# Kernel tuning notes

Measured on AMD Instinct MI355X. Metric: run time of the kernel, lower is better.

The kernel has to match this reference:

```python
import jax, jax.numpy as jnp
import numpy as np

HEADS = 8
DIM_HEAD = 64
SCALE = DIM_HEAD ** -0.5


def setup_inputs() -> dict:
    key = jax.random.key(0)
    ks = jax.random.split(key, 6)
    b, n, d = 2, 4096, 1024
    inner = HEADS * DIM_HEAD  # 512
    x = jax.random.normal(ks[0], (b, n, d), dtype=jnp.float32)
    Wq = jax.random.normal(ks[1], (d, inner), dtype=jnp.float32) * (d ** -0.5)
    Wk = jax.random.normal(ks[2], (d, inner), dtype=jnp.float32) * (d ** -0.5)
    Wv = jax.random.normal(ks[3], (d, inner), dtype=jnp.float32) * (d ** -0.5)
    Wout = jax.random.normal(ks[4], (inner, d), dtype=jnp.float32) * (inner ** -0.5)
    bout = jnp.zeros((d,), dtype=jnp.float32)
    return {"x": x, "Wq": Wq, "Wk": Wk, "Wv": Wv, "Wout": Wout, "bout": bout}


def reference(x, Wq, Wk, Wv, Wout, bout):
    b, n, _ = x.shape
    h, dh = HEADS, DIM_HEAD
    # self-attention: context = x
    q = (x @ Wq).reshape(b, n, h, dh).transpose(0, 2, 1, 3)  # b h n d
    k = (x @ Wk).reshape(b, n, h, dh).transpose(0, 2, 1, 3)
    v = (x @ Wv).reshape(b, n, h, dh).transpose(0, 2, 1, 3)
    sim = jnp.einsum('bhid,bhjd->bhij', q, k) * SCALE  # full score matrix
    attn = jax.nn.softmax(sim, axis=-1)
    out = jnp.einsum('bhij,bhjd->bhid', attn, v)
    out = out.transpose(0, 2, 1, 3).reshape(b, n, h * dh)  # b n (h d)
    return out @ Wout + bout
```

## Files before the change

### kernel.cpp

```cpp
#include <hip/hip_runtime.h>
#include <hip/hip_bf16.h>

typedef __bf16 bf16x8 __attribute__((ext_vector_type(8)));
typedef __bf16 bf16x4 __attribute__((ext_vector_type(4)));
typedef float floatx4 __attribute__((ext_vector_type(4)));

#define MFMA16(a, b, c) __builtin_amdgcn_mfma_f32_16x16x32_bf16((a), (b), (c), 0, 0, 0)

__device__ __forceinline__ void stage16(const __bf16* g, __bf16* lds_base) {
  __builtin_amdgcn_global_load_lds(
      (__attribute__((address_space(1))) void*)(void*)g,
      (__attribute__((address_space(3))) void*)lds_base, 16, 0, 0);
}

__global__ void detect_dtype(const unsigned int* __restrict__ x, int* __restrict__ flag) {
  __shared__ int cnt;
  if (threadIdx.x == 0) cnt = 0;
  __syncthreads();
  int c = 0;
  for (int i = threadIdx.x; i < 4096; i += 256) {
    const unsigned f = (x[i] >> 7) & 0xFF;
    c += (f >= 100 && f <= 140) ? 1 : 0;
  }
  atomicAdd(&cnt, c);
  __syncthreads();
  if (threadIdx.x == 0) *flag = (cnt > 2048) ? 1 : 0;
}

__global__ __launch_bounds__(256) void convert_x(const void* __restrict__ src,
                                                 __bf16* __restrict__ dst,
                                                 const int* __restrict__ flagp) {
  const int isbf = *flagp;
  const size_t i = ((size_t)blockIdx.x * 256 + threadIdx.x) * 8;
  if (isbf) {
    *(bf16x8*)(dst + i) = *(const bf16x8*)((const __bf16*)src + i);
  } else {
    const float4 f0 = *(const float4*)((const float*)src + i);
    const float4 f1 = *(const float4*)((const float*)src + i + 4);
    bf16x8 v;
    v[0] = (__bf16)f0.x; v[1] = (__bf16)f0.y; v[2] = (__bf16)f0.z; v[3] = (__bf16)f0.w;
    v[4] = (__bf16)f1.x; v[5] = (__bf16)f1.y; v[6] = (__bf16)f1.z; v[7] = (__bf16)f1.w;
    *(bf16x8*)(dst + i) = v;
  }
}

__global__ __launch_bounds__(256) void transpose3_conv(
    const void* __restrict__ s0, const void* __restrict__ s1,
    const void* __restrict__ s2, __bf16* __restrict__ dst,
    int R, int C, const int* __restrict__ flagp) {
  __shared__ __bf16 t[32][33];
  const int isbf = *flagp;
  const void* src = (blockIdx.z == 0) ? s0 : (blockIdx.z == 1) ? s1 : s2;
  __bf16* d = dst + (size_t)blockIdx.z * R * C;
  const int bx = blockIdx.x * 32, by = blockIdx.y * 32;
  const int x = threadIdx.x & 31, y0 = threadIdx.x >> 5;
#pragma unroll
  for (int i = y0; i < 32; i += 8) {
    const size_t idx = (size_t)(by + i) * C + bx + x;
    t[i][x] = isbf ? ((const __bf16*)src)[idx] : (__bf16)(((const float*)src)[idx]);
  }
  __syncthreads();
#pragma unroll
  for (int i = y0; i < 32; i += 8) d[(size_t)(bx + i) * R + by + x] = t[x][i];
}

__global__ __launch_bounds__(256) void transpose_conv(const void* __restrict__ src,
                                                      __bf16* __restrict__ dst,
                                                      int R, int C,
                                                      const int* __restrict__ flagp) {
  __shared__ __bf16 t[32][33];
  const int isbf = *flagp;
  const int bx = blockIdx.x * 32, by = blockIdx.y * 32;
  const int x = threadIdx.x & 31, y0 = threadIdx.x >> 5;
#pragma unroll
  for (int i = y0; i < 32; i += 8) {
    const size_t idx = (size_t)(by + i) * C + bx + x;
    t[i][x] = isbf ? ((const __bf16*)src)[idx] : (__bf16)(((const float*)src)[idx]);
  }
  __syncthreads();
#pragma unroll
  for (int i = y0; i < 32; i += 8) dst[(size_t)(bx + i) * R + by + x] = t[x][i];
}

__global__ __launch_bounds__(256) void vp_transpose(const __bf16* __restrict__ V,
                                                    __bf16* __restrict__ VP) {
  alignas(16) __shared__ __bf16 t[64][64];
  const int bh = blockIdx.y, s0 = blockIdx.x * 64;
  const int row = threadIdx.x >> 2, part = threadIdx.x & 3;
  const __bf16* src = V + (size_t)bh * 262144 + (size_t)(s0 + row) * 64 + part * 16;
  *(bf16x8*)&t[row][part * 16] = *(const bf16x8*)src;
  *(bf16x8*)&t[row][part * 16 + 8] = *(const bf16x8*)(src + 8);
  __syncthreads();
  const int d = row, og = part;
  bf16x8 w0, w1;
#pragma unroll
  for (int e = 0; e < 8; e++) {
    const int o0 = og * 16 + e, o1 = og * 16 + 8 + e;
    w0[e] = t[(o0 & 3) * 16 + (o0 >> 2)][d];
    w1[e] = t[(o1 & 3) * 16 + (o1 >> 2)][d];
  }
  __bf16* dst = VP + (size_t)bh * 262144 + (size_t)d * 4096 + s0 + og * 16;
  *(bf16x8*)dst = w0;
  *(bf16x8*)(dst + 8) = w1;
}

__global__ __launch_bounds__(256) void gemm_bt(
    const __bf16* __restrict__ A, const __bf16* __restrict__ Bt,
    void* __restrict__ Cv, void* __restrict__ Cv2, int M, int N, int K,
    const void* __restrict__ bias, int permute, int egress_dual,
    size_t zsB, size_t zsC, const int* __restrict__ flagp) {
  alignas(16) __shared__ __bf16 As[128 * 32];
  alignas(16) __shared__ __bf16 Bs[128 * 32];
  const int isbf = *flagp;
  Bt += blockIdx.z * zsB;
  const size_t zoff = (size_t)blockIdx.z * zsC;
  const int tid = threadIdx.x;
  const int wave = tid >> 6, lane = tid & 63;
  const int m0 = blockIdx.y * 128, n0 = blockIdx.x * 128;
  const int wm = (wave & 1) * 64, wn = (wave >> 1) * 64;
  const int fr = lane & 15, fq = lane >> 4;

  const floatx4 zero4 = {0.f, 0.f, 0.f, 0.f};
  floatx4 acc[4][4];
#pragma unroll
  for (int i = 0; i < 4; i++)
#pragma unroll
    for (int j = 0; j < 4; j++) acc[i][j] = zero4;

  const int lrow = lane >> 2;
  const int lk = (lane & 3) * 8;

  for (int k0 = 0; k0 < K; k0 += 32) {
#pragma unroll
    for (int cc = 0; cc < 2; ++cc) {
      const int c = 2 * wave + cc;
      stage16(A + (size_t)(m0 + c * 16 + lrow) * K + k0 + lk, &As[c * 512]);
      stage16(Bt + (size_t)(n0 + c * 16 + lrow) * K + k0 + lk, &Bs[c * 512]);
    }
    __syncthreads();
    bf16x8 af[4], bg[4];
#pragma unroll
    for (int mt = 0; mt < 4; mt++)
      af[mt] = *(const bf16x8*)&As[(wm + mt * 16 + fr) * 32 + fq * 8];
#pragma unroll
    for (int nt = 0; nt < 4; nt++)
      bg[nt] = *(const bf16x8*)&Bs[(wn + nt * 16 + fr) * 32 + fq * 8];
#pragma unroll
    for (int mt = 0; mt < 4; mt++)
#pragma unroll
      for (int nt = 0; nt < 4; nt++)
        acc[mt][nt] = MFMA16(af[mt], bg[nt], acc[mt][nt]);
    __syncthreads();
  }

  const float qs = (permute && blockIdx.z == 0) ? 0.18033688011112042f
                                                : 1.0f;
#pragma unroll
  for (int mt = 0; mt < 4; mt++)
#pragma unroll
    for (int nt = 0; nt < 4; nt++)
#pragma unroll
      for (int r = 0; r < 4; r++) {
        const int row = m0 + wm + mt * 16 + fq * 4 + r;
        const int col = n0 + wn + nt * 16 + fr;
        float v = acc[mt][nt][r] * qs;
        if (bias)
          v += isbf ? (float)((const __bf16*)bias)[col] : ((const float*)bias)[col];
        if (permute) {
          const int bh = (row >> 12) * 8 + (col >> 6);
          const int s = row & 4095, d = col & 63;
          const size_t pidx = (size_t)bh * 262144 + (size_t)s * 64 + d;
          if (blockIdx.z == 2)
            ((__bf16*)Cv2)[pidx] = (__bf16)v;
          else
            ((__bf16*)Cv)[zoff + pidx] = (__bf16)v;
        } else {
          const size_t idx = (size_t)row * N + col;
          if (egress_dual && !isbf)
            ((float*)Cv)[idx] = v;
          else
            ((__bf16*)Cv)[idx] = (__bf16)v;
        }
      }
}

#define ATT_S 4096
#define KV_SPLIT 2
__global__ __launch_bounds__(512, 4) void attn_flash(
    const __bf16* __restrict__ Qa, const __bf16* __restrict__ Ka,
    const __bf16* __restrict__ VPa, float* __restrict__ Of,
    float* __restrict__ lp) {
  alignas(16) __shared__ __bf16 Kl[2][64 * 64];
  alignas(16) __shared__ __bf16 Vl[2][64 * 64];
  alignas(16) __shared__ __bf16 Pl[8 * 32 * 64];
  const int tid = threadIdx.x, wave = tid >> 6, lane = tid & 63;
  const int bh = blockIdx.y, b = bh >> 3, h = bh & 7;
  const int z = blockIdx.z;
  const int q0 = blockIdx.x * 256 + wave * 32;
  const int fr = lane & 15, fq = lane >> 4;
  const __bf16* Qb = Qa + (size_t)bh * ATT_S * 64;
  const __bf16* Kb = Ka + (size_t)bh * ATT_S * 64;
  const __bf16* Vb = VPa + (size_t)bh * ATT_S * 64;

  const int sw0 = ((fq ^ (fr & 7)) * 8);
  const int sw1 = (((fq + 4) ^ (fr & 7)) * 8);
  const int r0 = tid >> 3;
  const int ssw = (((tid & 7) ^ (r0 & 7)) * 8);

  bf16x8 aq[2][2];
#pragma unroll
  for (int mt = 0; mt < 2; mt++)
#pragma unroll
    for (int kt = 0; kt < 2; kt++)
      aq[mt][kt] = *(const bf16x8*)(Qb + (size_t)(q0 + mt * 16 + fr) * 64 + kt * 32 + fq * 8);

  const floatx4 zero4 = {0.f, 0.f, 0.f, 0.f};
  floatx4 o[2][4];
  float lsum[2][4];
#pragma unroll
  for (int mt = 0; mt < 2; mt++) {
#pragma unroll
    for (int nt = 0; nt < 4; nt++) o[mt][nt] = zero4;
#pragma unroll
    for (int r = 0; r < 4; r++) lsum[mt][r] = 0.f;
  }

  const int JT = (ATT_S / 64) / KV_SPLIT;
  const int jbase = z * JT;

  stage16(Kb + (size_t)(jbase * 64 + r0) * 64 + ssw, &Kl[0][wave * 512]);
  stage16(Vb + (size_t)r0 * 4096 + jbase * 64 + ssw, &Vl[0][wave * 512]);

  for (int j = 0; j < JT; ++j) {
    __syncthreads();
    const int cur = j & 1;
    if (j + 1 < JT) {
      const int kv1 = (jbase + j + 1) * 64;
      stage16(Kb + (size_t)(kv1 + r0) * 64 + ssw, &Kl[1 - cur][wave * 512]);
      stage16(Vb + (size_t)r0 * 4096 + kv1 + ssw, &Vl[1 - cur][wave * 512]);
    }
    const __bf16* Klc = Kl[cur];
    const __bf16* Vlc = Vl[cur];

    floatx4 s4[2][4];
    __builtin_amdgcn_s_setprio(1);
#pragma unroll
    for (int nt = 0; nt < 4; nt++) {
      bf16x8 bk0 = *(const bf16x8*)&Klc[(nt * 16 + fr) * 64 + sw0];
      bf16x8 bk1 = *(const bf16x8*)&Klc[(nt * 16 + fr) * 64 + sw1];
#pragma unroll
      for (int mt = 0; mt < 2; mt++) {
        floatx4 zz = zero4;
        zz = MFMA16(aq[mt][0], bk0, zz);
        zz = MFMA16(aq[mt][1], bk1, zz);
        s4[mt][nt] = zz;
      }
    }
    __builtin_amdgcn_s_setprio(0);

#pragma unroll
    for (int mt = 0; mt < 2; mt++)
#pragma unroll
      for (int r = 0; r < 4; r++) {
        bf16x4 pv;
        float psum = 0.f;
#pragma unroll
        for (int nt = 0; nt < 4; nt++) {
          const float p = __builtin_amdgcn_exp2f(s4[mt][nt][r]);
          pv[nt] = (__bf16)p;
          psum += p;
        }
        lsum[mt][r] += psum;
        const int row = wave * 32 + mt * 16 + fq * 4 + r;
        const int vg = (fr >> 1) ^ ((fq * 4 + r) & 7);
        *(bf16x4*)&Pl[row * 64 + vg * 8 + (fr & 1) * 4] = pv;
      }
    asm volatile("s_waitcnt lgkmcnt(0)" ::: "memory");

    bf16x8 bv[4][2];
#pragma unroll
    for (int nt = 0; nt < 4; nt++) {
      bv[nt][0] = *(const bf16x8*)&Vlc[(nt * 16 + fr) * 64 + sw0];
      bv[nt][1] = *(const bf16x8*)&Vlc[(nt * 16 + fr) * 64 + sw1];
    }
    __builtin_amdgcn_s_setprio(1);
#pragma unroll
    for (int mt = 0; mt < 2; mt++) {
      const int prow = (wave * 32 + mt * 16 + fr) * 64;
      bf16x8 ap0 = *(const bf16x8*)&Pl[prow + sw0];
      bf16x8 ap1 = *(const bf16x8*)&Pl[prow + sw1];
#pragma unroll
      for (int nt = 0; nt < 4; nt++) {
        o[mt][nt] = MFMA16(ap0, bv[nt][0], o[mt][nt]);
        o[mt][nt] = MFMA16(ap1, bv[nt][1], o[mt][nt]);
      }
    }
    __builtin_amdgcn_s_setprio(0);
  }

#pragma unroll
  for (int off = 1; off < 16; off <<= 1)
#pragma unroll
    for (int mt = 0; mt < 2; mt++)
#pragma unroll
      for (int r = 0; r < 4; r++) lsum[mt][r] += __shfl_xor(lsum[mt][r], off, 64);

  float* Ofz = Of + (size_t)z * 8192 * 512;
  float* lz = lp + (size_t)z * 16 * 4096;
#pragma unroll
  for (int mt = 0; mt < 2; mt++)
#pragma unroll
    for (int r = 0; r < 4; r++) {
      const int row = q0 + mt * 16 + fq * 4 + r;
      if (fr == 0) lz[bh * 4096 + row] = lsum[mt][r];
#pragma unroll
      for (int nt = 0; nt < 4; nt++) {
        const int col = h * 64 + nt * 16 + fr;
        Ofz[(size_t)(b * ATT_S + row) * 512 + col] = o[mt][nt][r];
      }
    }
}

__global__ __launch_bounds__(256) void attn_combine(
    const float* __restrict__ Of, const float* __restrict__ lp,
    __bf16* __restrict__ O) {
  const size_t i = ((size_t)blockIdx.x * 256 + threadIdx.x) * 8;
  const int row = (int)(i >> 9), colb = (int)(i & 511);
  const int bh = (row >> 12) * 8 + (colb >> 6), qrow = row & 4095;
  const float l = lp[bh * 4096 + qrow] + lp[16 * 4096 + bh * 4096 + qrow];
  const float inv = 1.0f / l;
  const float4 a0 = *(const float4*)(Of + i);
  const float4 a1 = *(const float4*)(Of + i + 4);
  const float4 b0 = *(const float4*)(Of + 8192 * 512 + i);
  const float4 b1 = *(const float4*)(Of + 8192 * 512 + i + 4);
  bf16x8 w;
  w[0] = (__bf16)((a0.x + b0.x) * inv); w[1] = (__bf16)((a0.y + b0.y) * inv);
  w[2] = (__bf16)((a0.z + b0.z) * inv); w[3] = (__bf16)((a0.w + b0.w) * inv);
  w[4] = (__bf16)((a1.x + b1.x) * inv); w[5] = (__bf16)((a1.y + b1.y) * inv);
  w[6] = (__bf16)((a1.z + b1.z) * inv); w[7] = (__bf16)((a1.w + b1.w) * inv);
  *(bf16x8*)(O + i) = w;
}

extern "C" void kernel_launch(void* const* d_in, const int* in_sizes, int n_in,
                              void* d_out, int out_size, void* d_ws, size_t ws_size,
                              hipStream_t stream) {
  (void)in_sizes; (void)n_in; (void)out_size; (void)ws_size;
  const void* x = d_in[0];
  const void* Wq = d_in[1];
  const void* Wk = d_in[2];
  const void* Wv = d_in[3];
  const void* Wout = d_in[4];
  const void* bout = d_in[5];

  char* ws = (char*)d_ws;
  int* flag = (int*)ws;
  __bf16* wtq = (__bf16*)(ws + (1u << 20));
  __bf16* wto = (__bf16*)(ws + (4u << 20));
  __bf16* Q = (__bf16*)(ws + (5u << 20));
  __bf16* K = (__bf16*)(ws + (13u << 20));
  __bf16* VP = (__bf16*)(ws + (21u << 20));
  __bf16* O = (__bf16*)(ws + (29u << 20));
  __bf16* Vtmp = O;
  float* Of = (float*)(ws + (38u << 20));
  float* lp = (float*)(ws + (72u << 20));
  __bf16* xbf = (__bf16*)Of;

  detect_dtype<<<1, 256, 0, stream>>>((const unsigned int*)x, flag);

  transpose3_conv<<<dim3(16, 32, 3), 256, 0, stream>>>(Wq, Wk, Wv, wtq, 1024, 512, flag);
  transpose_conv<<<dim3(32, 16), 256, 0, stream>>>(Wout, wto, 512, 1024, flag);

  convert_x<<<4096, 256, 0, stream>>>(x, xbf, flag);

  gemm_bt<<<dim3(4, 64, 3), 256, 0, stream>>>(
      xbf, wtq, Q, Vtmp, 8192, 512, 1024, nullptr, 1, 0,
      (size_t)512 * 1024, (size_t)8192 * 512, flag);

  vp_transpose<<<dim3(64, 16), 256, 0, stream>>>(Vtmp, VP);

  attn_flash<<<dim3(ATT_S / 256, 16, KV_SPLIT), 512, 0, stream>>>(Q, K, VP, Of, lp);

  attn_combine<<<2048, 256, 0, stream>>>(Of, lp, O);

  gemm_bt<<<dim3(8, 64, 1), 256, 0, stream>>>(
      O, wto, d_out, nullptr, 8192, 1024, 512, bout, 0, 1, 0, 0, flag);
}
```

Before: 258.7 us.

## Double-buffer GEMM LDS tiles and hoist V fragment loads in attention loop

The projection GEMM now keeps two LDS buffers for the A and B tiles and prefetches the next K-slice with global_load_lds while the current slice feeds the MFMAs. It waits with explicit vmcnt counts and raw s_barrier instead of full __syncthreads. The attention loop issues its V fragment LDS reads before the QK^T MFMAs so their latency overlaps compute. The cost is doubled GEMM shared memory, which may lower occupancy, and more live registers in the attention loop.

```diff
diff --git a/kernel.cpp b/kernel.cpp
--- a/kernel.cpp
+++ b/kernel.cpp
@@ -109,8 +109,8 @@
     void* __restrict__ Cv, void* __restrict__ Cv2, int M, int N, int K,
     const void* __restrict__ bias, int permute, int egress_dual,
     size_t zsB, size_t zsC, const int* __restrict__ flagp) {
-  alignas(16) __shared__ __bf16 As[128 * 32];
-  alignas(16) __shared__ __bf16 Bs[128 * 32];
+  alignas(16) __shared__ __bf16 As[2][128 * 32];
+  alignas(16) __shared__ __bf16 Bs[2][128 * 32];
   const int isbf = *flagp;
   Bt += blockIdx.z * zsB;
   const size_t zoff = (size_t)blockIdx.z * zsC;
@@ -129,28 +129,45 @@
 
   const int lrow = lane >> 2;
   const int lk = (lane & 3) * 8;
-
-  for (int k0 = 0; k0 < K; k0 += 32) {
-#pragma unroll
-    for (int cc = 0; cc < 2; ++cc) {
-      const int c = 2 * wave + cc;
-      stage16(A + (size_t)(m0 + c * 16 + lrow) * K + k0 + lk, &As[c * 512]);
-      stage16(Bt + (size_t)(n0 + c * 16 + lrow) * K + k0 + lk, &Bs[c * 512]);
-    }
-    __syncthreads();
+  const int NT = K >> 5;
+
+#pragma unroll
+  for (int cc = 0; cc < 2; ++cc) {
+    const int c = 2 * wave + cc;
+    stage16(A + (size_t)(m0 + c * 16 + lrow) * K + lk, &As[0][c * 512]);
+    stage16(Bt + (size_t)(n0 + c * 16 + lrow) * K + lk, &Bs[0][c * 512]);
+  }
+
+  for (int t = 0; t < NT; ++t) {
+    const int cur = t & 1;
+    if (t + 1 < NT) {
+      const int k1 = (t + 1) << 5;
+#pragma unroll
+      for (int cc = 0; cc < 2; ++cc) {
+        const int c = 2 * wave + cc;
+        stage16(A + (size_t)(m0 + c * 16 + lrow) * K + k1 + lk, &As[1 - cur][c * 512]);
+        stage16(Bt + (size_t)(n0 + c * 16 + lrow) * K + k1 + lk, &Bs[1 - cur][c * 512]);
+      }
+      asm volatile("s_waitcnt vmcnt(4)" ::: "memory");
+    } else {
+      asm volatile("s_waitcnt vmcnt(0)" ::: "memory");
+    }
+    __builtin_amdgcn_s_barrier();
+    __builtin_amdgcn_sched_barrier(0);
     bf16x8 af[4], bg[4];
 #pragma unroll
     for (int mt = 0; mt < 4; mt++)
-      af[mt] = *(const bf16x8*)&As[(wm + mt * 16 + fr) * 32 + fq * 8];
+      af[mt] = *(const bf16x8*)&As[cur][(wm + mt * 16 + fr) * 32 + fq * 8];
 #pragma unroll
     for (int nt = 0; nt < 4; nt++)
-      bg[nt] = *(const bf16x8*)&Bs[(wn + nt * 16 + fr) * 32 + fq * 8];
+      bg[nt] = *(const bf16x8*)&Bs[cur][(wn + nt * 16 + fr) * 32 + fq * 8];
 #pragma unroll
     for (int mt = 0; mt < 4; mt++)
 #pragma unroll
       for (int nt = 0; nt < 4; nt++)
         acc[mt][nt] = MFMA16(af[mt], bg[nt], acc[mt][nt]);
-    __syncthreads();
+    __builtin_amdgcn_sched_barrier(0);
+    __builtin_amdgcn_s_barrier();
   }
 
   const float qs = (permute && blockIdx.z == 0) ? 0.18033688011112042f
@@ -242,6 +259,13 @@
     const __bf16* Klc = Kl[cur];
     const __bf16* Vlc = Vl[cur];
 
+    bf16x8 bv[4][2];
+#pragma unroll
+    for (int nt = 0; nt < 4; nt++) {
+      bv[nt][0] = *(const bf16x8*)&Vlc[(nt * 16 + fr) * 64 + sw0];
+      bv[nt][1] = *(const bf16x8*)&Vlc[(nt * 16 + fr) * 64 + sw1];
+    }
+
     floatx4 s4[2][4];
     __builtin_amdgcn_s_setprio(1);
 #pragma unroll
@@ -277,12 +301,6 @@
       }
     asm volatile("s_waitcnt lgkmcnt(0)" ::: "memory");
 
-    bf16x8 bv[4][2];
-#pragma unroll
-    for (int nt = 0; nt < 4; nt++) {
-      bv[nt][0] = *(const bf16x8*)&Vlc[(nt * 16 + fr) * 64 + sw0];
-      bv[nt][1] = *(const bf16x8*)&Vlc[(nt * 16 + fr) * 64 + sw1];
-    }
     __builtin_amdgcn_s_setprio(1);
 #pragma unroll
     for (int mt = 0; mt < 2; mt++) {
```

Measured after the change: 380.1 us. 1.47x slower.
